# Kernel optimization log

Hardware: AMD Instinct MI355X
Metric: run time of the kernel (lower is better)

Reference implementation:

```python
import jax, jax.numpy as jnp
import numpy as np

NUM_HEADS = 16
NEG_INF = -1e18


def setup_inputs() -> dict:
    key = jax.random.key(0)
    ks = jax.random.split(key, 9)
    T, B, D = 2048, 2, 1024
    s = 1.0 / np.sqrt(D)
    return {
        "query": jax.random.normal(ks[0], (T, B, D), jnp.float32),
        "q_w": jax.random.normal(ks[1], (D, D), jnp.float32) * s,
        "q_b": jax.random.normal(ks[2], (D,), jnp.float32) * 0.02,
        "k_w": jax.random.normal(ks[3], (D, D), jnp.float32) * s,
        "k_b": jax.random.normal(ks[4], (D,), jnp.float32) * 0.02,
        "v_w": jax.random.normal(ks[5], (D, D), jnp.float32) * s,
        "v_b": jax.random.normal(ks[6], (D,), jnp.float32) * 0.02,
        "out_w": jax.random.normal(ks[7], (D, D), jnp.float32) * s,
        "out_b": jax.random.normal(ks[8], (D,), jnp.float32) * 0.02,
    }


def reference(query, q_w, q_b, k_w, k_b, v_w, v_b, out_w, out_b):
    # query: [T, B, D] (Time x Batch x Channel). Self-attention, causal mask,
    # dropout=0, need_weights=True.
    T, B, D = query.shape
    H = NUM_HEADS
    hd = D // H
    scaling = 1.0 / jnp.sqrt(jnp.asarray(hd, query.dtype))

    q = (query @ q_w.T + q_b) * scaling
    k = query @ k_w.T + k_b
    v = query @ v_w.T + v_b

    def split_heads(x):  # [T, B, D] -> [B, H, T, hd]
        return x.reshape(T, B, H, hd).transpose(1, 2, 0, 3)

    qh, kh, vh = split_heads(q), split_heads(k), split_heads(v)

    # scores: [B, H, T, T]
    scores = jnp.einsum("bhtd,bhsd->bhts", qh, kh)
    causal = jnp.triu(jnp.full((T, T), NEG_INF, dtype=scores.dtype), k=1)
    scores = scores + causal

    probs = jax.nn.softmax(scores, axis=-1)
    attn = jnp.einsum("bhts,bhsd->bhtd", probs, vh)  # [B, H, T, hd]
    attn = attn.transpose(2, 0, 1, 3).reshape(T, B, D)
    out = attn @ out_w.T + out_b

    # averaged attention weights over heads: [B, T, T]
    avg_weights = probs.sum(axis=1) / H
    return out, avg_weights
```

## Files before the change

kernel.cpp:

```cpp
#include <hip/hip_runtime.h>
#include <hip/hip_bf16.h>
#include <stdint.h>

typedef __hip_bfloat16 bf16;
using short8 = __attribute__((ext_vector_type(8))) short;
using f32x4  = __attribute__((ext_vector_type(4))) float;

#define TDIM 2048
#define BDIM 2
#define DDIM 1024
#define HNUM 16
#define HD   64
#define MDIM 4096
#define M0   16.0f

__device__ __forceinline__ f32x4 mfma16(short8 a, short8 b, f32x4 c) {
  return __builtin_amdgcn_mfma_f32_16x16x32_bf16(a, b, c, 0, 0, 0);
}

union S8 { short8 v; bf16 h[8]; };

__global__ __launch_bounds__(256) void cast_all_kernel(
    const float* __restrict__ q, const float* __restrict__ wq,
    const float* __restrict__ wk, const float* __restrict__ wv,
    const float* __restrict__ wo, bf16* __restrict__ dst) {
  int t4 = blockIdx.x * blockDim.x + threadIdx.x;
  int idx = t4 * 4;
  const float* s;
  if (idx < 4194304)      s = q  + idx;
  else if (idx < 5242880) s = wq + (idx - 4194304);
  else if (idx < 6291456) s = wk + (idx - 5242880);
  else if (idx < 7340032) s = wv + (idx - 6291456);
  else                    s = wo + (idx - 7340032);
  float4 v = *(const float4*)s;
  union { ushort4 u; bf16 b[4]; } pk;
  pk.b[0] = __float2bfloat16(v.x);
  pk.b[1] = __float2bfloat16(v.y);
  pk.b[2] = __float2bfloat16(v.z);
  pk.b[3] = __float2bfloat16(v.w);
  *(ushort4*)(dst + idx) = pk.u;
}

__global__ __launch_bounds__(256) void qkv_kernel(
    const bf16* __restrict__ X, const bf16* __restrict__ Wq,
    const bf16* __restrict__ Wk, const bf16* __restrict__ Wv,
    const float* __restrict__ qb, const float* __restrict__ kb,
    const float* __restrict__ vb, bf16* __restrict__ Qo,
    bf16* __restrict__ Ko, bf16* __restrict__ Vto) {
  __shared__ bf16 Xs[64][40];
  __shared__ bf16 Qs[64][40];
  __shared__ bf16 Ks[64][40];
  __shared__ bf16 Vs[64][40];
  const int tid  = threadIdx.x;
  const int lane = tid & 63, wave = tid >> 6;
  const int m0 = blockIdx.y * 64, n0 = blockIdx.x * 64;
  const int wm = (wave >> 1) * 32, wn = (wave & 1) * 32;
  const int fr = lane & 15, quad = lane >> 4, q8 = quad * 8;
  const int ldr = tid >> 2, ldc = (tid & 3) * 8;
  f32x4 aq[2][2] = {}, ak[2][2] = {}, av[2][2] = {};
  const bf16* xptr = X  + (size_t)(m0 + ldr) * DDIM + ldc;
  const bf16* qptr = Wq + (size_t)(n0 + ldr) * DDIM + ldc;
  const bf16* kptr = Wk + (size_t)(n0 + ldr) * DDIM + ldc;
  const bf16* vptr = Wv + (size_t)(n0 + ldr) * DDIM + ldc;
  for (int k0 = 0; k0 < DDIM; k0 += 32) {
    uint4 xv = *(const uint4*)(xptr + k0);
    uint4 qv = *(const uint4*)(qptr + k0);
    uint4 kv = *(const uint4*)(kptr + k0);
    uint4 vv = *(const uint4*)(vptr + k0);
    __syncthreads();
    *(uint4*)&Xs[ldr][ldc] = xv;
    *(uint4*)&Qs[ldr][ldc] = qv;
    *(uint4*)&Ks[ldr][ldc] = kv;
    *(uint4*)&Vs[ldr][ldc] = vv;
    __syncthreads();
    short8 xf[2], qf[2], kf[2], vf[2];
    xf[0] = *(const short8*)&Xs[wm + fr][q8];
    xf[1] = *(const short8*)&Xs[wm + 16 + fr][q8];
    qf[0] = *(const short8*)&Qs[wn + fr][q8];
    qf[1] = *(const short8*)&Qs[wn + 16 + fr][q8];
    kf[0] = *(const short8*)&Ks[wn + fr][q8];
    kf[1] = *(const short8*)&Ks[wn + 16 + fr][q8];
    vf[0] = *(const short8*)&Vs[wn + fr][q8];
    vf[1] = *(const short8*)&Vs[wn + 16 + fr][q8];
#pragma unroll
    for (int i = 0; i < 2; i++)
#pragma unroll
      for (int j = 0; j < 2; j++) {
        aq[i][j] = mfma16(xf[i], qf[j], aq[i][j]);
        ak[i][j] = mfma16(xf[i], kf[j], ak[i][j]);
        av[i][j] = mfma16(vf[i], xf[j], av[i][j]);
      }
  }
#pragma unroll
  for (int mt = 0; mt < 2; mt++)
#pragma unroll
    for (int nt = 0; nt < 2; nt++)
#pragma unroll
      for (int i = 0; i < 4; i++) {
        {
          int gm = m0 + wm + mt * 16 + quad * 4 + i;
          int gn = n0 + wn + nt * 16 + fr;
          int t = gm >> 1, b = gm & 1, h = gn >> 6, e = gn & 63;
          size_t o = ((size_t)(b * HNUM + h) * TDIM + t) * HD + e;
          Qo[o] = __float2bfloat16((aq[mt][nt][i] + qb[gn]) * 0.125f);
          Ko[o] = __float2bfloat16(ak[mt][nt][i] + kb[gn]);
        }
        {
          int gf = n0 + wn + mt * 16 + quad * 4 + i;
          int gt = m0 + wm + nt * 16 + fr;
          int t = gt >> 1, b = gt & 1, h = gf >> 6, e = gf & 63;
          Vto[((size_t)(b * HNUM + h) * HD + e) * TDIM + t] =
              __float2bfloat16(av[mt][nt][i] + vb[gf]);
        }
      }
}

__global__ __launch_bounds__(256) void gemm_out_kernel(
    const bf16* __restrict__ A, const bf16* __restrict__ Bw,
    const float* __restrict__ bias, float* __restrict__ of32) {
  __shared__ bf16 As[64][40];
  __shared__ bf16 Bs[64][40];
  const int tid  = threadIdx.x;
  const int lane = tid & 63, wave = tid >> 6;
  const int m0 = blockIdx.y * 64, n0 = blockIdx.x * 64;
  const int wm = (wave >> 1) * 32, wn = (wave & 1) * 32;
  const int fr = lane & 15, quad = lane >> 4, q8 = quad * 8;
  const int ldr = tid >> 2, ldc = (tid & 3) * 8;
  f32x4 acc[2][2] = {};
  const bf16* aptr = A  + (size_t)(m0 + ldr) * DDIM + ldc;
  const bf16* bptr = Bw + (size_t)(n0 + ldr) * DDIM + ldc;
  for (int k0 = 0; k0 < DDIM; k0 += 32) {
    uint4 avv = *(const uint4*)(aptr + k0);
    uint4 bvv = *(const uint4*)(bptr + k0);
    __syncthreads();
    *(uint4*)&As[ldr][ldc] = avv;
    *(uint4*)&Bs[ldr][ldc] = bvv;
    __syncthreads();
    short8 af[2], bfr[2];
    af[0]  = *(const short8*)&As[wm + fr][q8];
    af[1]  = *(const short8*)&As[wm + 16 + fr][q8];
    bfr[0] = *(const short8*)&Bs[wn + fr][q8];
    bfr[1] = *(const short8*)&Bs[wn + 16 + fr][q8];
    acc[0][0] = mfma16(af[0], bfr[0], acc[0][0]);
    acc[0][1] = mfma16(af[0], bfr[1], acc[0][1]);
    acc[1][0] = mfma16(af[1], bfr[0], acc[1][0]);
    acc[1][1] = mfma16(af[1], bfr[1], acc[1][1]);
  }
#pragma unroll
  for (int mt = 0; mt < 2; mt++)
#pragma unroll
    for (int nt = 0; nt < 2; nt++)
#pragma unroll
      for (int i = 0; i < 4; i++) {
        int gm = m0 + wm + mt * 16 + quad * 4 + i;
        int gn = n0 + wn + nt * 16 + fr;
        of32[(size_t)gm * DDIM + gn] = acc[mt][nt][i] + bias[gn];
      }
}

__global__ __launch_bounds__(256) void attn_split_kernel(
    const bf16* __restrict__ Q, const bf16* __restrict__ K,
    const bf16* __restrict__ Vt, bf16* __restrict__ P0o,
    bf16* __restrict__ P1o, float* __restrict__ l0buf,
    float* __restrict__ l1buf) {
  __shared__ bf16 Ks[2][64][40];
  __shared__ bf16 Vs[2][64][40];
  __shared__ bf16 pt[4][16][72];
  const int tid = threadIdx.x, lane = tid & 63, wave = tid >> 6;
  const int bid = blockIdx.x;
  const int part = bid & 1, bh = (bid >> 1) & 31, t64 = 31 - (bid >> 6);
  const int b = bh >> 4, h = bh & 15;
  const int t0 = t64 * 64 + wave * 16;
  const int fr = lane & 15, quad = lane >> 4, q8 = quad * 8;
  const bf16* Qp = Q + ((size_t)bh * TDIM + t0) * HD;
  const bf16* Kp = K + (size_t)bh * TDIM * HD;
  const bf16* Vp = Vt + (size_t)bh * HD * TDIM;
  short8 aq0 = *(const short8*)&Qp[fr * HD + q8];
  short8 aq1 = *(const short8*)&Qp[fr * HD + 32 + q8];
  const int Cb = t64 + 1, C0 = Cb >> 1;
  const int clo = part ? C0 : 0, chi = part ? Cb : C0;
  const int sr0 = tid >> 3, scc = (tid & 7) * 8, sr1 = sr0 + 32;
  const int ssub = scc >> 5, scol = scc & 31;
  f32x4 oacc[4] = {};
  float lsum[4] = {0.f, 0.f, 0.f, 0.f};
  uint4 kv0, kv1, vv0, vv1;
  auto ldglob = [&](int c) {
    int s0 = c * 64;
    kv0 = *(const uint4*)&Kp[(size_t)(s0 + sr0) * HD + scc];
    kv1 = *(const uint4*)&Kp[(size_t)(s0 + sr1) * HD + scc];
    vv0 = *(const uint4*)&Vp[(size_t)sr0 * TDIM + s0 + scc];
    vv1 = *(const uint4*)&Vp[(size_t)sr1 * TDIM + s0 + scc];
  };
  if (clo < chi) ldglob(clo);
  for (int c = clo; c < chi; c++) {
    __syncthreads();
    *(uint4*)&Ks[ssub][sr0][scol] = kv0;
    *(uint4*)&Ks[ssub][sr1][scol] = kv1;
    *(uint4*)&Vs[ssub][sr0][scol] = vv0;
    *(uint4*)&Vs[ssub][sr1][scol] = vv1;
    __syncthreads();
    if (c + 1 < chi) ldglob(c + 1);
    const int s0 = c * 64;
    f32x4 sc[4] = {};
#pragma unroll
    for (int j = 0; j < 4; j++) {
      short8 b0 = *(const short8*)&Ks[0][j * 16 + fr][q8];
      short8 b1 = *(const short8*)&Ks[1][j * 16 + fr][q8];
      sc[j] = mfma16(aq0, b0, sc[j]);
      sc[j] = mfma16(aq1, b1, sc[j]);
    }
#pragma unroll
    for (int j = 0; j < 4; j++) {
      int s_col = s0 + j * 16 + fr;
#pragma unroll
      for (int i = 0; i < 4; i++) {
        float p = 0.f;
        if (s_col <= t0 + quad * 4 + i) {
          p = __expf(sc[j][i] - M0);
          lsum[i] += p;
        }
        pt[wave][quad * 4 + i][j * 16 + fr] = __float2bfloat16(p);
      }
    }
    short8 ap0 = *(const short8*)&pt[wave][fr][q8];
    short8 ap1 = *(const short8*)&pt[wave][fr][32 + q8];
#pragma unroll
    for (int nt = 0; nt < 4; nt++) {
      short8 v0 = *(const short8*)&Vs[0][nt * 16 + fr][q8];
      short8 v1 = *(const short8*)&Vs[1][nt * 16 + fr][q8];
      oacc[nt] = mfma16(ap0, v0, oacc[nt]);
      oacc[nt] = mfma16(ap1, v1, oacc[nt]);
    }
  }
  float lr[4];
#pragma unroll
  for (int i = 0; i < 4; i++) {
    float l = lsum[i];
#pragma unroll
    for (int off = 1; off < 16; off <<= 1) l += __shfl_xor(l, off, 16);
    lr[i] = l;
  }
  bf16*  Op = part ? P1o : P0o;
  float* lb = part ? l1buf : l0buf;
#pragma unroll
  for (int nt = 0; nt < 4; nt++)
#pragma unroll
    for (int i = 0; i < 4; i++) {
      int t_row = t0 + quad * 4 + i;
      int col = h * HD + nt * 16 + fr;
      Op[((size_t)t_row * BDIM + b) * DDIM + col] = __float2bfloat16(oacc[nt][i]);
    }
  if (fr == 0) {
    float4 v = make_float4(lr[0], lr[1], lr[2], lr[3]);
    *(float4*)&lb[(size_t)bh * TDIM + t0 + quad * 4] = v;
  }
}

__global__ __launch_bounds__(256) void combine_kernel(
    const bf16* __restrict__ P0, bf16* __restrict__ Ab,
    const float* __restrict__ l0buf, const float* __restrict__ l1buf,
    float* __restrict__ invl) {
  int idx = (blockIdx.x * 256 + threadIdx.x) * 8;
  int t = idx >> 11, b = (idx >> 10) & 1, d = idx & 1023, h = d >> 6;
  int bh = b * HNUM + h;
  size_t li = (size_t)bh * TDIM + t;
  float inv = 1.0f / (l0buf[li] + l1buf[li]);
  S8 a, c, o;
  a.v = *(const short8*)&P0[idx];
  c.v = *(const short8*)&Ab[idx];
#pragma unroll
  for (int k = 0; k < 8; k++)
    o.h[k] = __float2bfloat16(
        (__bfloat162float(a.h[k]) + __bfloat162float(c.h[k])) * inv);
  *(short8*)&Ab[idx] = o.v;
  if ((d & 63) == 0) invl[li] = inv;
}

__global__ __launch_bounds__(256) void avg_kernel(
    const bf16* __restrict__ Q, const bf16* __restrict__ K,
    const float* __restrict__ invl_ws, float* __restrict__ avgw) {
  const int tid = threadIdx.x;
  int r = blockIdx.x;
  const int b = (r >= 2048) ? 1 : 0;
  r &= 2047;
  float* avp = avgw + (size_t)b * TDIM * TDIM;
  if (r >= 1056) {
    int r2 = r - 1056;
    int ti = 0;
    while (ti < 31 && (ti + 1) * (62 - ti) <= r2) ti++;
    int si = (2 * ti + 2) + (r2 - ti * (63 - ti));
    int t0b = ti * 64, s0 = si * 32;
#pragma unroll
    for (int k = 0; k < 2; k++) {
      int off = (tid * 2 + k) * 4;
      *(float4*)&avp[(size_t)(t0b + (off >> 5)) * TDIM + s0 + (off & 31)] =
          make_float4(0.f, 0.f, 0.f, 0.f);
    }
    return;
  }
  int ti = 0;
  while ((ti + 1) * (ti + 2) <= r) ti++;
  const int si = r - ti * (ti + 1);
  const int t0b = ti * 64, s0 = si * 32;

  __shared__ bf16 Qs[2][64][40];
  __shared__ bf16 Ks2[2][32][40];
  __shared__ float sinvl[HNUM][64];
#pragma unroll
  for (int k = 0; k < 4; k++) {
    int idx = tid + k * 256;
    sinvl[idx >> 6][idx & 63] =
        invl_ws[(size_t)(b * HNUM + (idx >> 6)) * TDIM + t0b + (idx & 63)];
  }
  const int lane = tid & 63, wave = tid >> 6;
  const int fr = lane & 15, quad = lane >> 4, q8 = quad * 8;
  const int twr = wave * 16;
  const int qr0 = tid >> 3, qcc = (tid & 7) * 8, qr1 = qr0 + 32;
  const int qsub = qcc >> 5, qcol = qcc & 31;
  const bf16* Qb = Q + (size_t)b * HNUM * TDIM * HD;
  const bf16* Kb = K + (size_t)b * HNUM * TDIM * HD;
  uint4 qv0, qv1, kv1;
  auto ldh = [&](int hh) {
    const bf16* Qh = Qb + (size_t)hh * TDIM * HD;
    const bf16* Kh = Kb + (size_t)hh * TDIM * HD;
    qv0 = *(const uint4*)&Qh[(size_t)(t0b + qr0) * HD + qcc];
    qv1 = *(const uint4*)&Qh[(size_t)(t0b + qr1) * HD + qcc];
    kv1 = *(const uint4*)&Kh[(size_t)(s0 + (qr0 & 31)) * HD + qcc];
  };
  ldh(0);
  f32x4 facc[2] = {};
  for (int hh = 0; hh < HNUM; hh++) {
    __syncthreads();
    *(uint4*)&Qs[qsub][qr0][qcol] = qv0;
    *(uint4*)&Qs[qsub][qr1][qcol] = qv1;
    if (qr0 < 32) *(uint4*)&Ks2[qsub][qr0][qcol] = kv1;
    else          *(uint4*)&Ks2[qsub][qr0 - 32][qcol] = kv1;
    __syncthreads();
    if (hh + 1 < HNUM) ldh(hh + 1);
    short8 a0 = *(const short8*)&Qs[0][twr + fr][q8];
    short8 a1 = *(const short8*)&Qs[1][twr + fr][q8];
#pragma unroll
    for (int nt = 0; nt < 2; nt++) {
      short8 b0 = *(const short8*)&Ks2[0][nt * 16 + fr][q8];
      short8 b1 = *(const short8*)&Ks2[1][nt * 16 + fr][q8];
      f32x4 sc = {};
      sc = mfma16(a0, b0, sc);
      sc = mfma16(a1, b1, sc);
#pragma unroll
      for (int i = 0; i < 4; i++) {
        int tr = twr + quad * 4 + i;
        if (s0 + nt * 16 + fr <= t0b + tr)
          facc[nt][i] += __expf(sc[i] - M0) * sinvl[hh][tr];
      }
    }
  }
#pragma unroll
  for (int nt = 0; nt < 2; nt++)
#pragma unroll
    for (int i = 0; i < 4; i++)
      avp[(size_t)(t0b + twr + quad * 4 + i) * TDIM + s0 + nt * 16 + fr] =
          facc[nt][i] * 0.0625f;
}

extern "C" void kernel_launch(void* const* d_in, const int* in_sizes, int n_in,
                              void* d_out, int out_size, void* d_ws, size_t ws_size,
                              hipStream_t stream) {
  const float* q   = (const float*)d_in[0];
  const float* q_w = (const float*)d_in[1];
  const float* q_b = (const float*)d_in[2];
  const float* k_w = (const float*)d_in[3];
  const float* k_b = (const float*)d_in[4];
  const float* v_w = (const float*)d_in[5];
  const float* v_b = (const float*)d_in[6];
  const float* o_w = (const float*)d_in[7];
  const float* o_b = (const float*)d_in[8];
  float* out = (float*)d_out;
  float* avg = out + (size_t)MDIM * DDIM;

  bf16* ws  = (bf16*)d_ws;
  bf16* Xbf = ws;
  bf16* Wq  = ws + 4194304;
  bf16* Wk  = ws + 5242880;
  bf16* Wv  = ws + 6291456;
  bf16* Wo  = ws + 7340032;
  bf16* Qw  = ws + 8388608;
  bf16* Kw  = ws + 12582912;
  bf16* Vt  = ws + 16777216;
  bf16* Ab  = ws + 20971520;
  bf16* P0  = ws;
  float* l0   = (float*)(ws + 4194304);
  float* l1   = (float*)(ws + 4325376);
  float* invl = (float*)(ws + 4456448);

  cast_all_kernel<<<8192, 256, 0, stream>>>(q, q_w, k_w, v_w, o_w, Xbf);
  qkv_kernel<<<dim3(16, 64), 256, 0, stream>>>(Xbf, Wq, Wk, Wv, q_b, k_b, v_b,
                                               Qw, Kw, Vt);
  attn_split_kernel<<<2048, 256, 0, stream>>>(Qw, Kw, Vt, P0, Ab, l0, l1);
  combine_kernel<<<2048, 256, 0, stream>>>(P0, Ab, l0, l1, invl);
  avg_kernel<<<4096, 256, 0, stream>>>(Qw, Kw, invl, avg);
  gemm_out_kernel<<<dim3(16, 64), 256, 0, stream>>>(Ab, Wo, o_b, out);
}
```

Baseline: 261.9 us.

## Fuse split-attention combine into output GEMM and retile QKV with direct LDS loads

Removes the separate combine kernel. The output-projection GEMM now reads both partial attention outputs, sums them and normalises by the inverse softmax denominator while staging its A tile, and the averaging kernel recomputes the inverse denominator from l0/l1 itself. The QKV projection kernel moves to 128x64 tiles with a K step of 64 and uses global_load_lds to copy tiles straight into unpadded shared memory. This saves a full read and write pass over the attention output and raises reuse in QKV. The cost is extra ALU work in the GEMM load path, and the unpadded LDS rows may cause bank conflicts.

```diff
diff --git a/kernel.cpp b/kernel.cpp
--- a/kernel.cpp
+++ b/kernel.cpp
@@ -19,6 +19,12 @@
 }
 
 union S8 { short8 v; bf16 h[8]; };
+
+__device__ __forceinline__ void gload16(const bf16* g, bf16* l) {
+  __builtin_amdgcn_global_load_lds(
+      (const __attribute__((address_space(1))) unsigned int*)g,
+      (__attribute__((address_space(3))) unsigned int*)l, 16, 0, 0);
+}
 
 __global__ __launch_bounds__(256) void cast_all_kernel(
     const float* __restrict__ q, const float* __restrict__ wq,
@@ -47,93 +53,127 @@
     const float* __restrict__ qb, const float* __restrict__ kb,
     const float* __restrict__ vb, bf16* __restrict__ Qo,
     bf16* __restrict__ Ko, bf16* __restrict__ Vto) {
-  __shared__ bf16 Xs[64][40];
-  __shared__ bf16 Qs[64][40];
-  __shared__ bf16 Ks[64][40];
-  __shared__ bf16 Vs[64][40];
+  __shared__ bf16 Xs[128][64];
+  __shared__ bf16 Qs[64][64];
+  __shared__ bf16 Ks[64][64];
+  __shared__ bf16 Vs[64][64];
+  const int tid = threadIdx.x, lane = tid & 63, wave = tid >> 6;
+  const int m0 = blockIdx.y * 128, n0 = blockIdx.x * 64;
+  const int wm = (wave >> 1) * 64, wn = (wave & 1) * 32;
+  const int fr = lane & 15, quad = lane >> 4, q8 = quad * 8;
+  const int lr = lane >> 3, lc = (lane & 7) * 8;
+  f32x4 aq[4][2] = {}, ak[4][2] = {}, av[2][4] = {};
+  for (int k0 = 0; k0 < DDIM; k0 += 64) {
+    if (k0) __syncthreads();
+#pragma unroll
+    for (int p = 0; p < 10; p++) {
+      int pid = wave * 10 + p;
+      const bf16* g;
+      bf16* l;
+      if (pid < 16) {
+        g = X + (size_t)(m0 + pid * 8 + lr) * DDIM + k0 + lc;
+        l = &Xs[pid * 8][0];
+      } else if (pid < 24) {
+        int r = (pid - 16) * 8;
+        g = Wq + (size_t)(n0 + r + lr) * DDIM + k0 + lc;
+        l = &Qs[r][0];
+      } else if (pid < 32) {
+        int r = (pid - 24) * 8;
+        g = Wk + (size_t)(n0 + r + lr) * DDIM + k0 + lc;
+        l = &Ks[r][0];
+      } else {
+        int r = (pid - 32) * 8;
+        g = Wv + (size_t)(n0 + r + lr) * DDIM + k0 + lc;
+        l = &Vs[r][0];
+      }
+      gload16(g, l);
+    }
+    __syncthreads();
+#pragma unroll
+    for (int kk = 0; kk < 2; kk++) {
+      const int ko = kk * 32 + q8;
+      short8 xf[4], qf[2], kf[2], vf[2];
+#pragma unroll
+      for (int i = 0; i < 4; i++)
+        xf[i] = *(const short8*)&Xs[wm + i * 16 + fr][ko];
+#pragma unroll
+      for (int j = 0; j < 2; j++) {
+        qf[j] = *(const short8*)&Qs[wn + j * 16 + fr][ko];
+        kf[j] = *(const short8*)&Ks[wn + j * 16 + fr][ko];
+        vf[j] = *(const short8*)&Vs[wn + j * 16 + fr][ko];
+      }
+#pragma unroll
+      for (int i = 0; i < 4; i++)
+#pragma unroll
+        for (int j = 0; j < 2; j++) {
+          aq[i][j] = mfma16(xf[i], qf[j], aq[i][j]);
+          ak[i][j] = mfma16(xf[i], kf[j], ak[i][j]);
+          av[j][i] = mfma16(vf[j], xf[i], av[j][i]);
+        }
+    }
+  }
+#pragma unroll
+  for (int i = 0; i < 4; i++)
+#pragma unroll
+    for (int j = 0; j < 2; j++)
+#pragma unroll
+      for (int r = 0; r < 4; r++) {
+        {
+          int gm = m0 + wm + i * 16 + quad * 4 + r;
+          int gn = n0 + wn + j * 16 + fr;
+          int t = gm >> 1, bb = gm & 1, h = gn >> 6, e = gn & 63;
+          size_t o = ((size_t)(bb * HNUM + h) * TDIM + t) * HD + e;
+          Qo[o] = __float2bfloat16((aq[i][j][r] + qb[gn]) * 0.125f);
+          Ko[o] = __float2bfloat16(ak[i][j][r] + kb[gn]);
+        }
+        {
+          int gf = n0 + wn + j * 16 + quad * 4 + r;
+          int gt = m0 + wm + i * 16 + fr;
+          int t = gt >> 1, bb = gt & 1, h = gf >> 6, e = gf & 63;
+          Vto[((size_t)(bb * HNUM + h) * HD + e) * TDIM + t] =
+              __float2bfloat16(av[j][i][r] + vb[gf]);
+        }
+      }
+}
+
+__global__ __launch_bounds__(256) void gemm_out_kernel(
+    const bf16* __restrict__ P0, const bf16* __restrict__ P1,
+    const bf16* __restrict__ Bw, const float* __restrict__ l0buf,
+    const float* __restrict__ l1buf, const float* __restrict__ bias,
+    float* __restrict__ of32) {
+  __shared__ bf16 As[64][40];
+  __shared__ bf16 Bs[64][40];
+  __shared__ float sInv[64][16];
   const int tid  = threadIdx.x;
   const int lane = tid & 63, wave = tid >> 6;
   const int m0 = blockIdx.y * 64, n0 = blockIdx.x * 64;
   const int wm = (wave >> 1) * 32, wn = (wave & 1) * 32;
   const int fr = lane & 15, quad = lane >> 4, q8 = quad * 8;
   const int ldr = tid >> 2, ldc = (tid & 3) * 8;
-  f32x4 aq[2][2] = {}, ak[2][2] = {}, av[2][2] = {};
-  const bf16* xptr = X  + (size_t)(m0 + ldr) * DDIM + ldc;
-  const bf16* qptr = Wq + (size_t)(n0 + ldr) * DDIM + ldc;
-  const bf16* kptr = Wk + (size_t)(n0 + ldr) * DDIM + ldc;
-  const bf16* vptr = Wv + (size_t)(n0 + ldr) * DDIM + ldc;
-  for (int k0 = 0; k0 < DDIM; k0 += 32) {
-    uint4 xv = *(const uint4*)(xptr + k0);
-    uint4 qv = *(const uint4*)(qptr + k0);
-    uint4 kv = *(const uint4*)(kptr + k0);
-    uint4 vv = *(const uint4*)(vptr + k0);
-    __syncthreads();
-    *(uint4*)&Xs[ldr][ldc] = xv;
-    *(uint4*)&Qs[ldr][ldc] = qv;
-    *(uint4*)&Ks[ldr][ldc] = kv;
-    *(uint4*)&Vs[ldr][ldc] = vv;
-    __syncthreads();
-    short8 xf[2], qf[2], kf[2], vf[2];
-    xf[0] = *(const short8*)&Xs[wm + fr][q8];
-    xf[1] = *(const short8*)&Xs[wm + 16 + fr][q8];
-    qf[0] = *(const short8*)&Qs[wn + fr][q8];
-    qf[1] = *(const short8*)&Qs[wn + 16 + fr][q8];
-    kf[0] = *(const short8*)&Ks[wn + fr][q8];
-    kf[1] = *(const short8*)&Ks[wn + 16 + fr][q8];
-    vf[0] = *(const short8*)&Vs[wn + fr][q8];
-    vf[1] = *(const short8*)&Vs[wn + 16 + fr][q8];
-#pragma unroll
-    for (int i = 0; i < 2; i++)
-#pragma unroll
-      for (int j = 0; j < 2; j++) {
-        aq[i][j] = mfma16(xf[i], qf[j], aq[i][j]);
-        ak[i][j] = mfma16(xf[i], kf[j], ak[i][j]);
-        av[i][j] = mfma16(vf[i], xf[j], av[i][j]);
-      }
-  }
-#pragma unroll
-  for (int mt = 0; mt < 2; mt++)
-#pragma unroll
-    for (int nt = 0; nt < 2; nt++)
-#pragma unroll
-      for (int i = 0; i < 4; i++) {
-        {
-          int gm = m0 + wm + mt * 16 + quad * 4 + i;
-          int gn = n0 + wn + nt * 16 + fr;
-          int t = gm >> 1, b = gm & 1, h = gn >> 6, e = gn & 63;
-          size_t o = ((size_t)(b * HNUM + h) * TDIM + t) * HD + e;
-          Qo[o] = __float2bfloat16((aq[mt][nt][i] + qb[gn]) * 0.125f);
-          Ko[o] = __float2bfloat16(ak[mt][nt][i] + kb[gn]);
-        }
-        {
-          int gf = n0 + wn + mt * 16 + quad * 4 + i;
-          int gt = m0 + wm + nt * 16 + fr;
-          int t = gt >> 1, b = gt & 1, h = gf >> 6, e = gf & 63;
-          Vto[((size_t)(b * HNUM + h) * HD + e) * TDIM + t] =
-              __float2bfloat16(av[mt][nt][i] + vb[gf]);
-        }
-      }
-}
-
-__global__ __launch_bounds__(256) void gemm_out_kernel(
-    const bf16* __restrict__ A, const bf16* __restrict__ Bw,
-    const float* __restrict__ bias, float* __restrict__ of32) {
-  __shared__ bf16 As[64][40];
-  __shared__ bf16 Bs[64][40];
-  const int tid  = threadIdx.x;
-  const int lane = tid & 63, wave = tid >> 6;
-  const int m0 = blockIdx.y * 64, n0 = blockIdx.x * 64;
-  const int wm = (wave >> 1) * 32, wn = (wave & 1) * 32;
-  const int fr = lane & 15, quad = lane >> 4, q8 = quad * 8;
-  const int ldr = tid >> 2, ldc = (tid & 3) * 8;
+#pragma unroll
+  for (int e = 0; e < 4; e++) {
+    int idx = tid * 4 + e;
+    int row = idx >> 4, h = idx & 15;
+    int gm = m0 + row, t = gm >> 1, bb = gm & 1;
+    size_t li = (size_t)(bb * HNUM + h) * TDIM + t;
+    sInv[row][h] = 1.0f / (l0buf[li] + l1buf[li]);
+  }
+  __syncthreads();
   f32x4 acc[2][2] = {};
-  const bf16* aptr = A  + (size_t)(m0 + ldr) * DDIM + ldc;
+  const size_t arow = (size_t)(m0 + ldr) * DDIM + ldc;
   const bf16* bptr = Bw + (size_t)(n0 + ldr) * DDIM + ldc;
   for (int k0 = 0; k0 < DDIM; k0 += 32) {
-    uint4 avv = *(const uint4*)(aptr + k0);
+    S8 a0, a1, apk;
+    a0.v = *(const short8*)&P0[arow + k0];
+    a1.v = *(const short8*)&P1[arow + k0];
     uint4 bvv = *(const uint4*)(bptr + k0);
-    __syncthreads();
-    *(uint4*)&As[ldr][ldc] = avv;
+    float inv = sInv[ldr][k0 >> 6];
+#pragma unroll
+    for (int k = 0; k < 8; k++)
+      apk.h[k] = __float2bfloat16(
+          (__bfloat162float(a0.h[k]) + __bfloat162float(a1.h[k])) * inv);
+    __syncthreads();
+    *(short8*)&As[ldr][ldc] = apk.v;
     *(uint4*)&Bs[ldr][ldc] = bvv;
     __syncthreads();
     short8 af[2], bfr[2];
@@ -256,29 +296,10 @@
   }
 }
 
-__global__ __launch_bounds__(256) void combine_kernel(
-    const bf16* __restrict__ P0, bf16* __restrict__ Ab,
-    const float* __restrict__ l0buf, const float* __restrict__ l1buf,
-    float* __restrict__ invl) {
-  int idx = (blockIdx.x * 256 + threadIdx.x) * 8;
-  int t = idx >> 11, b = (idx >> 10) & 1, d = idx & 1023, h = d >> 6;
-  int bh = b * HNUM + h;
-  size_t li = (size_t)bh * TDIM + t;
-  float inv = 1.0f / (l0buf[li] + l1buf[li]);
-  S8 a, c, o;
-  a.v = *(const short8*)&P0[idx];
-  c.v = *(const short8*)&Ab[idx];
-#pragma unroll
-  for (int k = 0; k < 8; k++)
-    o.h[k] = __float2bfloat16(
-        (__bfloat162float(a.h[k]) + __bfloat162float(c.h[k])) * inv);
-  *(short8*)&Ab[idx] = o.v;
-  if ((d & 63) == 0) invl[li] = inv;
-}
-
 __global__ __launch_bounds__(256) void avg_kernel(
     const bf16* __restrict__ Q, const bf16* __restrict__ K,
-    const float* __restrict__ invl_ws, float* __restrict__ avgw) {
+    const float* __restrict__ l0buf, const float* __restrict__ l1buf,
+    float* __restrict__ avgw) {
   const int tid = threadIdx.x;
   int r = blockIdx.x;
   const int b = (r >= 2048) ? 1 : 0;
@@ -309,8 +330,8 @@
 #pragma unroll
   for (int k = 0; k < 4; k++) {
     int idx = tid + k * 256;
-    sinvl[idx >> 6][idx & 63] =
-        invl_ws[(size_t)(b * HNUM + (idx >> 6)) * TDIM + t0b + (idx & 63)];
+    size_t li = (size_t)(b * HNUM + (idx >> 6)) * TDIM + t0b + (idx & 63);
+    sinvl[idx >> 6][idx & 63] = 1.0f / (l0buf[li] + l1buf[li]);
   }
   const int lane = tid & 63, wave = tid >> 6;
   const int fr = lane & 15, quad = lane >> 4, q8 = quad * 8;
@@ -386,17 +407,15 @@
   bf16* Qw  = ws + 8388608;
   bf16* Kw  = ws + 12582912;
   bf16* Vt  = ws + 16777216;
-  bf16* Ab  = ws + 20971520;
+  bf16* P1  = ws + 20971520;
   bf16* P0  = ws;
-  float* l0   = (float*)(ws + 4194304);
-  float* l1   = (float*)(ws + 4325376);
-  float* invl = (float*)(ws + 4456448);
+  float* l0 = (float*)(ws + 4194304);
+  float* l1 = (float*)(ws + 4325376);
 
   cast_all_kernel<<<8192, 256, 0, stream>>>(q, q_w, k_w, v_w, o_w, Xbf);
-  qkv_kernel<<<dim3(16, 64), 256, 0, stream>>>(Xbf, Wq, Wk, Wv, q_b, k_b, v_b,
+  qkv_kernel<<<dim3(16, 32), 256, 0, stream>>>(Xbf, Wq, Wk, Wv, q_b, k_b, v_b,
                                                Qw, Kw, Vt);
-  attn_split_kernel<<<2048, 256, 0, stream>>>(Qw, Kw, Vt, P0, Ab, l0, l1);
-  combine_kernel<<<2048, 256, 0, stream>>>(P0, Ab, l0, l1, invl);
-  avg_kernel<<<4096, 256, 0, stream>>>(Qw, Kw, invl, avg);
-  gemm_out_kernel<<<dim3(16, 64), 256, 0, stream>>>(Ab, Wo, o_b, out);
-}
+  attn_split_kernel<<<2048, 256, 0, stream>>>(Qw, Kw, Vt, P0, P1, l0, l1);
+  avg_kernel<<<4096, 256, 0, stream>>>(Qw, Kw, l0, l1, avg);
+  gemm_out_kernel<<<dim3(16, 64), 256, 0, stream>>>(P0, P1, Wo, l0, l1, o_b, out);
+}
```

New measurement: 265.4 us. No clear change (+1.3%).
